# Kernel tuning notes

Hardware: AMD Instinct MI355X
Metric: run time of the kernel (lower is better)

The kernel has to match this reference:

```python
import jax, jax.numpy as jnp
import numpy as np

BATCH, IN, OUT, P = 8192, 1024, 1024, 8

def setup_inputs() -> dict:
    key = jax.random.key(0)
    k1, k2, k3 = jax.random.split(key, 3)
    x = jax.random.normal(k1, (BATCH, IN), dtype=jnp.float32)
    # per-(output,input) basis coefficients, init ~ randn*0.1 as in torch module
    coefficients = jax.random.normal(k2, (OUT, IN, P), dtype=jnp.float32) * 0.1
    weights = jax.random.normal(k3, (OUT, IN), dtype=jnp.float32)
    return {"x": x, "coefficients": coefficients, "weights": weights}

def reference(x, coefficients, weights):
    # out[b,o] = sum_i x[b,i] * (sum_p coef[o,i,p]) * weights[o,i]
    # == x @ (coef_sum * weights)^T  -- single fused GEMM
    w_eff = coefficients.sum(axis=-1) * weights  # [O, I]
    return jnp.einsum('bi,oi->bo', x, w_eff)
```

## Files before the change

kernel.cpp:

```cpp
#include <hip/hip_runtime.h>
#include <hip/hip_bf16.h>
#include <stdint.h>

#define BATCH 8192
#define IN    1024
#define OUTD  1024
#define PBASIS 8

typedef __attribute__((ext_vector_type(8))) short bf16x8;
typedef __attribute__((ext_vector_type(4))) float floatx4;

__device__ __forceinline__ unsigned short f2bf(float f) {
    union { float f; unsigned u; } v; v.f = f;
    unsigned u = v.u;
    u += 0x7fffu + ((u >> 16) & 1u);
    return (unsigned short)(u >> 16);
}

__global__ void weff_kernel(const float* __restrict__ coef,
                            const float* __restrict__ w,
                            unsigned short* __restrict__ weff) {
    int idx = blockIdx.x * blockDim.x + threadIdx.x;
    size_t e0 = (size_t)idx * 2;
    const float4* c4 = (const float4*)(coef + e0 * PBASIS);
    float4 a = c4[0], b = c4[1], c = c4[2], d = c4[3];
    float s0 = (a.x + a.y + a.z + a.w) + (b.x + b.y + b.z + b.w);
    float s1 = (c.x + c.y + c.z + c.w) + (d.x + d.y + d.z + d.w);
    float2 ww = ((const float2*)w)[idx];
    unsigned b0 = f2bf(s0 * ww.x);
    unsigned b1 = f2bf(s1 * ww.y);
    ((unsigned*)weff)[idx] = b0 | (b1 << 16);
}

__global__ void cvtx_kernel(const float* __restrict__ x, unsigned short* __restrict__ xb) {
    int idx = blockIdx.x * blockDim.x + threadIdx.x;
    const float4* p = (const float4*)(x + (size_t)idx * 8);
    float4 a = p[0], b = p[1];
    uint4 o;
    o.x = (unsigned)f2bf(a.x) | ((unsigned)f2bf(a.y) << 16);
    o.y = (unsigned)f2bf(a.z) | ((unsigned)f2bf(a.w) << 16);
    o.z = (unsigned)f2bf(b.x) | ((unsigned)f2bf(b.y) << 16);
    o.w = (unsigned)f2bf(b.z) | ((unsigned)f2bf(b.w) << 16);
    ((uint4*)xb)[idx] = o;
}

__global__ __launch_bounds__(256, 2) void gemm_bt(
        const unsigned short* __restrict__ A,
        const unsigned short* __restrict__ B,
        float* __restrict__ C) {
    constexpr int K = IN, BM = 128, BN = 128, BK = 32;
    __shared__ unsigned short As[BM * BK];
    __shared__ unsigned short Bs[BN * BK];

    const int tid  = threadIdx.x;
    const int bm   = blockIdx.x, bn = blockIdx.y;
    const int lane = tid & 63;
    const int wave = tid >> 6;
    const int wm   = wave & 1, wn = wave >> 1;
    const int t    = lane & 15;
    const int q    = lane >> 4;
    const int sw   = (t >> 1) & 3;

    const char* gA[2]; const char* gB[2];
    void* lA[2]; void* lB[2];
#pragma unroll
    for (int j = 0; j < 2; ++j) {
        int L = j * 256 + tid;
        int row = L >> 2;
        int cg  = (L & 3) ^ ((row >> 1) & 3);
        gA[j] = (const char*)(A + ((size_t)(bm * BM + row)) * K + cg * 8);
        gB[j] = (const char*)(B + ((size_t)(bn * BN + row)) * K + cg * 8);
        lA[j] = (void*)(As + (size_t)L * 8);
        lB[j] = (void*)(Bs + (size_t)L * 8);
    }

    const bf16x8* aptr[4]; const bf16x8* bptr[4];
#pragma unroll
    for (int i = 0; i < 4; ++i) {
        int rowa = wm * 64 + i * 16 + t;
        int rowb = wn * 64 + i * 16 + t;
        aptr[i] = (const bf16x8*)(As + rowa * BK + ((q ^ sw) * 8));
        bptr[i] = (const bf16x8*)(Bs + rowb * BK + ((q ^ sw) * 8));
    }

    floatx4 acc[4][4];
#pragma unroll
    for (int i = 0; i < 4; ++i)
#pragma unroll
        for (int j = 0; j < 4; ++j)
            acc[i][j] = (floatx4){0.f, 0.f, 0.f, 0.f};

    for (int k0 = 0; k0 < K; k0 += BK) {
#pragma unroll
        for (int j = 0; j < 2; ++j) {
            __builtin_amdgcn_global_load_lds(
                (const __attribute__((address_space(1))) unsigned*)gA[j],
                (__attribute__((address_space(3))) unsigned*)lA[j], 16, 0, 0);
            __builtin_amdgcn_global_load_lds(
                (const __attribute__((address_space(1))) unsigned*)gB[j],
                (__attribute__((address_space(3))) unsigned*)lB[j], 16, 0, 0);
            gA[j] += BK * 2;
            gB[j] += BK * 2;
        }
        __syncthreads();

        bf16x8 af[4], bfv[4];
#pragma unroll
        for (int i = 0; i < 4; ++i) { af[i] = aptr[i][0]; bfv[i] = bptr[i][0]; }
#pragma unroll
        for (int i = 0; i < 4; ++i)
#pragma unroll
            for (int j = 0; j < 4; ++j)
                acc[i][j] = __builtin_amdgcn_mfma_f32_16x16x32_bf16(
                    af[i], bfv[j], acc[i][j], 0, 0, 0);
        __syncthreads();
    }

#pragma unroll
    for (int tm = 0; tm < 4; ++tm)
#pragma unroll
        for (int tn = 0; tn < 4; ++tn) {
            int col = bn * BN + wn * 64 + tn * 16 + t;
#pragma unroll
            for (int r = 0; r < 4; ++r) {
                int rowg = bm * BM + wm * 64 + tm * 16 + q * 4 + r;
                C[(size_t)rowg * OUTD + col] = acc[tm][tn][r];
            }
        }
}

extern "C" void kernel_launch(void* const* d_in, const int* in_sizes, int n_in,
                              void* d_out, int out_size, void* d_ws, size_t ws_size,
                              hipStream_t stream) {
    const float* x    = (const float*)d_in[0];
    const float* coef = (const float*)d_in[1];
    const float* w    = (const float*)d_in[2];
    float* out = (float*)d_out;

    unsigned short* xb   = (unsigned short*)d_ws;
    unsigned short* weff = (unsigned short*)((char*)d_ws + (size_t)BATCH * IN * 2);

    cvtx_kernel<<<(BATCH * IN / 8) / 256, 256, 0, stream>>>(x, xb);
    weff_kernel<<<(OUTD * IN / 2) / 256, 256, 0, stream>>>(coef, w, weff);
    gemm_bt<<<dim3(BATCH / 128, OUTD / 128), 256, 0, stream>>>(xb, weff, out);
}
```

Baseline: 129.9 us.

## Merge prep kernels, double GEMM K-tile, stage epilogue through LDS for coalesced stores

Combines the x-conversion and weight-fusion kernels into one launch, which saves a kernel launch. The GEMM K-tile goes from 32 to 64 with an 8-way XOR swizzle, halving the number of barrier pairs per K loop. The output is now staged through shared memory in two passes so each block writes full rows with float4 stores instead of scattered scalar stores. This adds extra barriers and LDS traffic in the epilogue, and the per-block LDS use stays within a budget that should still allow two blocks per CU.

```diff
diff --git a/kernel.cpp b/kernel.cpp
--- a/kernel.cpp
+++ b/kernel.cpp
@@ -17,40 +17,47 @@
     return (unsigned short)(u >> 16);
 }
 
-__global__ void weff_kernel(const float* __restrict__ coef,
+__global__ void prep_kernel(const float* __restrict__ x,
+                            const float* __restrict__ coef,
                             const float* __restrict__ w,
+                            unsigned short* __restrict__ xb,
                             unsigned short* __restrict__ weff) {
-    int idx = blockIdx.x * blockDim.x + threadIdx.x;
-    size_t e0 = (size_t)idx * 2;
-    const float4* c4 = (const float4*)(coef + e0 * PBASIS);
-    float4 a = c4[0], b = c4[1], c = c4[2], d = c4[3];
-    float s0 = (a.x + a.y + a.z + a.w) + (b.x + b.y + b.z + b.w);
-    float s1 = (c.x + c.y + c.z + c.w) + (d.x + d.y + d.z + d.w);
-    float2 ww = ((const float2*)w)[idx];
-    unsigned b0 = f2bf(s0 * ww.x);
-    unsigned b1 = f2bf(s1 * ww.y);
-    ((unsigned*)weff)[idx] = b0 | (b1 << 16);
-}
-
-__global__ void cvtx_kernel(const float* __restrict__ x, unsigned short* __restrict__ xb) {
-    int idx = blockIdx.x * blockDim.x + threadIdx.x;
-    const float4* p = (const float4*)(x + (size_t)idx * 8);
-    float4 a = p[0], b = p[1];
-    uint4 o;
-    o.x = (unsigned)f2bf(a.x) | ((unsigned)f2bf(a.y) << 16);
-    o.y = (unsigned)f2bf(a.z) | ((unsigned)f2bf(a.w) << 16);
-    o.z = (unsigned)f2bf(b.x) | ((unsigned)f2bf(b.y) << 16);
-    o.w = (unsigned)f2bf(b.z) | ((unsigned)f2bf(b.w) << 16);
-    ((uint4*)xb)[idx] = o;
+    int b = blockIdx.x;
+    int tid = threadIdx.x;
+    if (b < 4096) {
+        int idx = b * 256 + tid;
+        const float4* p = (const float4*)(x + (size_t)idx * 8);
+        float4 a = p[0], c = p[1];
+        uint4 o;
+        o.x = (unsigned)f2bf(a.x) | ((unsigned)f2bf(a.y) << 16);
+        o.y = (unsigned)f2bf(a.z) | ((unsigned)f2bf(a.w) << 16);
+        o.z = (unsigned)f2bf(c.x) | ((unsigned)f2bf(c.y) << 16);
+        o.w = (unsigned)f2bf(c.z) | ((unsigned)f2bf(c.w) << 16);
+        ((uint4*)xb)[idx] = o;
+    } else {
+        int idx = (b - 4096) * 256 + tid;
+        size_t e0 = (size_t)idx * 2;
+        const float4* c4 = (const float4*)(coef + e0 * PBASIS);
+        float4 a = c4[0], bb = c4[1], c = c4[2], d = c4[3];
+        float s0 = (a.x + a.y + a.z + a.w) + (bb.x + bb.y + bb.z + bb.w);
+        float s1 = (c.x + c.y + c.z + c.w) + (d.x + d.y + d.z + d.w);
+        float2 ww = ((const float2*)w)[idx];
+        unsigned b0 = f2bf(s0 * ww.x);
+        unsigned b1 = f2bf(s1 * ww.y);
+        ((unsigned*)weff)[idx] = b0 | (b1 << 16);
+    }
 }
 
 __global__ __launch_bounds__(256, 2) void gemm_bt(
         const unsigned short* __restrict__ A,
         const unsigned short* __restrict__ B,
         float* __restrict__ C) {
-    constexpr int K = IN, BM = 128, BN = 128, BK = 32;
-    __shared__ unsigned short As[BM * BK];
-    __shared__ unsigned short Bs[BN * BK];
+    constexpr int K = IN, BK = 64;
+    constexpr int ES = 132;
+    __shared__ __align__(16) char smem[64 * ES * 4];
+    unsigned short* As = (unsigned short*)smem;
+    unsigned short* Bs = As + 128 * BK;
+    float* ebuf = (float*)smem;
 
     const int tid  = threadIdx.x;
     const int bm   = blockIdx.x, bn = blockIdx.y;
@@ -59,29 +66,25 @@
     const int wm   = wave & 1, wn = wave >> 1;
     const int t    = lane & 15;
     const int q    = lane >> 4;
-    const int sw   = (t >> 1) & 3;
+    const int r8   = t & 7;
 
-    const char* gA[2]; const char* gB[2];
-    void* lA[2]; void* lB[2];
+    const char* gA[4]; const char* gB[4];
+    void* lA[4]; void* lB[4];
 #pragma unroll
-    for (int j = 0; j < 2; ++j) {
+    for (int j = 0; j < 4; ++j) {
         int L = j * 256 + tid;
-        int row = L >> 2;
-        int cg  = (L & 3) ^ ((row >> 1) & 3);
-        gA[j] = (const char*)(A + ((size_t)(bm * BM + row)) * K + cg * 8);
-        gB[j] = (const char*)(B + ((size_t)(bn * BN + row)) * K + cg * 8);
+        int row = L >> 3;
+        int cg  = (L & 7) ^ (row & 7);
+        gA[j] = (const char*)(A + ((size_t)(bm * 128 + row)) * K + cg * 8);
+        gB[j] = (const char*)(B + ((size_t)(bn * 128 + row)) * K + cg * 8);
         lA[j] = (void*)(As + (size_t)L * 8);
         lB[j] = (void*)(Bs + (size_t)L * 8);
     }
 
-    const bf16x8* aptr[4]; const bf16x8* bptr[4];
-#pragma unroll
-    for (int i = 0; i < 4; ++i) {
-        int rowa = wm * 64 + i * 16 + t;
-        int rowb = wn * 64 + i * 16 + t;
-        aptr[i] = (const bf16x8*)(As + rowa * BK + ((q ^ sw) * 8));
-        bptr[i] = (const bf16x8*)(Bs + rowb * BK + ((q ^ sw) * 8));
-    }
+    const unsigned short* aB0 = As + (wm * 64 + t) * BK + ((0 + q) ^ r8) * 8;
+    const unsigned short* aB1 = As + (wm * 64 + t) * BK + ((4 + q) ^ r8) * 8;
+    const unsigned short* bB0 = Bs + (wn * 64 + t) * BK + ((0 + q) ^ r8) * 8;
+    const unsigned short* bB1 = Bs + (wn * 64 + t) * BK + ((4 + q) ^ r8) * 8;
 
     floatx4 acc[4][4];
 #pragma unroll
@@ -92,7 +95,7 @@
 
     for (int k0 = 0; k0 < K; k0 += BK) {
 #pragma unroll
-        for (int j = 0; j < 2; ++j) {
+        for (int j = 0; j < 4; ++j) {
             __builtin_amdgcn_global_load_lds(
                 (const __attribute__((address_space(1))) unsigned*)gA[j],
                 (__attribute__((address_space(3))) unsigned*)lA[j], 16, 0, 0);
@@ -104,29 +107,53 @@
         }
         __syncthreads();
 
-        bf16x8 af[4], bfv[4];
+        bf16x8 af[2][4], bfv[2][4];
 #pragma unroll
-        for (int i = 0; i < 4; ++i) { af[i] = aptr[i][0]; bfv[i] = bptr[i][0]; }
+        for (int i = 0; i < 4; ++i) {
+            af[0][i]  = *(const bf16x8*)(aB0 + i * 1024);
+            af[1][i]  = *(const bf16x8*)(aB1 + i * 1024);
+            bfv[0][i] = *(const bf16x8*)(bB0 + i * 1024);
+            bfv[1][i] = *(const bf16x8*)(bB1 + i * 1024);
+        }
 #pragma unroll
         for (int i = 0; i < 4; ++i)
 #pragma unroll
-            for (int j = 0; j < 4; ++j)
+            for (int j = 0; j < 4; ++j) {
                 acc[i][j] = __builtin_amdgcn_mfma_f32_16x16x32_bf16(
-                    af[i], bfv[j], acc[i][j], 0, 0, 0);
+                    af[0][i], bfv[0][j], acc[i][j], 0, 0, 0);
+                acc[i][j] = __builtin_amdgcn_mfma_f32_16x16x32_bf16(
+                    af[1][i], bfv[1][j], acc[i][j], 0, 0, 0);
+            }
         __syncthreads();
     }
 
 #pragma unroll
-    for (int tm = 0; tm < 4; ++tm)
+    for (int p = 0; p < 2; ++p) {
+        if (p) __syncthreads();
 #pragma unroll
-        for (int tn = 0; tn < 4; ++tn) {
-            int col = bn * BN + wn * 64 + tn * 16 + t;
+        for (int dt = 0; dt < 2; ++dt) {
+            int tm = 2 * p + dt;
 #pragma unroll
-            for (int r = 0; r < 4; ++r) {
-                int rowg = bm * BM + wm * 64 + tm * 16 + q * 4 + r;
-                C[(size_t)rowg * OUTD + col] = acc[tm][tn][r];
+            for (int tn = 0; tn < 4; ++tn) {
+                int col = wn * 64 + tn * 16 + t;
+#pragma unroll
+                for (int r = 0; r < 4; ++r) {
+                    int brow = wm * 32 + dt * 16 + q * 4 + r;
+                    ebuf[brow * ES + col] = acc[tm][tn][r];
+                }
             }
         }
+        __syncthreads();
+#pragma unroll
+        for (int rr = 0; rr < 8; ++rr) {
+            int brow = rr * 8 + (tid >> 5);
+            int col4 = tid & 31;
+            float4 v = *(const float4*)(ebuf + brow * ES + col4 * 4);
+            int lrow = brow + ((brow >> 5) << 5) + p * 32;
+            size_t off = ((size_t)(bm * 128 + lrow) * OUTD + bn * 128 + col4 * 4);
+            *(float4*)(C + off) = v;
+        }
+    }
 }
 
 extern "C" void kernel_launch(void* const* d_in, const int* in_sizes, int n_in,
@@ -140,7 +167,6 @@
     unsigned short* xb   = (unsigned short*)d_ws;
     unsigned short* weff = (unsigned short*)((char*)d_ws + (size_t)BATCH * IN * 2);
 
-    cvtx_kernel<<<(BATCH * IN / 8) / 256, 256, 0, stream>>>(x, xb);
-    weff_kernel<<<(OUTD * IN / 2) / 256, 256, 0, stream>>>(coef, w, weff);
+    prep_kernel<<<6144, 256, 0, stream>>>(x, coef, w, xb, weff);
     gemm_bt<<<dim3(BATCH / 128, OUTD / 128), 256, 0, stream>>>(xb, weff, out);
 }
```

Result: faster. 125.7 us (-3.2%).
